# Optimization experiments

Hardware: AMD Instinct MI355X
Metric: run time of the kernel (lower is better)

The kernel has to match this reference:

```python
import jax, jax.numpy as jnp
import numpy as np

STRIDES = (8, 16, 32)
H = W = 640
SCORE_T = 0.5
NMS_T = 0.4


def setup_inputs() -> dict:
    key = jax.random.key(0)
    ks = jax.random.split(key, 9)
    feats = [(H // s) * (W // s) for s in STRIDES]  # 6400, 1600, 400
    d = {}
    for i, n in enumerate(feats):
        d[f"score{i}"] = jax.random.normal(ks[i], (1, n, 1), jnp.float32)
        d[f"bbox{i}"] = jax.random.normal(ks[3 + i], (1, n, 4), jnp.float32)
        d[f"kps{i}"] = jax.random.normal(ks[6 + i], (1, n, 10), jnp.float32)
    return d


def _anchors(stride):
    fh, fw = H // stride, W // stride
    yv, xv = jnp.meshgrid(jnp.arange(fh), jnp.arange(fw), indexing="ij")
    return jnp.stack([xv, yv], -1).reshape(-1, 2).astype(jnp.float32) * stride


def _decode(score, bbox, kps, stride):
    pts = _anchors(stride)                      # [N,2]
    s = jax.nn.sigmoid(score[0]).reshape(-1)    # [N]
    d = bbox[0] * stride                        # [N,4]
    x1 = pts[:, 0] - d[:, 0]
    y1 = pts[:, 1] - d[:, 1]
    x2 = pts[:, 0] + d[:, 2]
    y2 = pts[:, 1] + d[:, 3]
    b = jnp.stack([x1, y1, x2, y2], -1)         # [N,4]
    kd = (kps[0] * stride).reshape(-1, 5, 2)    # [N,5,2] (px,py pairs)
    k = (pts[:, None, :] + kd).reshape(-1, 10)  # [N,10]
    return s, b, k


def _iou(b):
    area = (b[:, 2] - b[:, 0]) * (b[:, 3] - b[:, 1])
    lt = jnp.maximum(b[:, None, :2], b[None, :, :2])
    rb = jnp.minimum(b[:, None, 2:], b[None, :, 2:])
    wh = jnp.clip(rb - lt, 0.0)
    inter = wh[..., 0] * wh[..., 1]
    return inter / (area[:, None] + area[None, :] - inter + 1e-9)


def _nms_keep(iou, valid, thresh):
    # greedy NMS on score-sorted boxes: keep i iff no earlier kept j has IoU>thresh
    n = valid.shape[0]
    def body(keep, xs):
        i, row = xs
        suppressed = jnp.any(keep & (row > thresh))
        keep = keep.at[i].set(valid[i] & ~suppressed)
        return keep, None
    keep, _ = jax.lax.scan(body, jnp.zeros(n, bool), (jnp.arange(n), iou))
    return keep


def reference(score0, score1, score2, bbox0, bbox1, bbox2, kps0, kps1, kps2):
    parts = [
        _decode(s, b, k, st)
        for s, b, k, st in zip(
            (score0, score1, score2), (bbox0, bbox1, bbox2), (kps0, kps1, kps2), STRIDES
        )
    ]
    scores = jnp.concatenate([p[0] for p in parts])  # [8400]
    boxes = jnp.concatenate([p[1] for p in parts])   # [8400,4]
    kpss = jnp.concatenate([p[2] for p in parts])    # [8400,10]
    order = jnp.argsort(-scores)                     # score-descending (NMS order)
    scores = scores[order]
    boxes = boxes[order]
    kpss = kpss[order]
    valid = scores > SCORE_T                         # threshold mask
    iou = _iou(jax.lax.stop_gradient(boxes))         # [8400,8400] ~282MB
    keep = _nms_keep(iou, valid, NMS_T)
    m = keep.astype(boxes.dtype)
    # fixed-shape equivalent of dynamic gather: suppressed rows zeroed, keep mask returned
    return boxes * m[:, None], scores * m, kpss * m[:, None], keep
```

## Files before the change

kernel.cpp:

```cpp
#include <hip/hip_runtime.h>
#include <math.h>

#define N_TOT 8400
#define MASK_WORDS 132
#define CAP 32
#define RT 33

typedef unsigned long long u64;

__device__ __forceinline__ unsigned mono_u32(float f) {
    unsigned u = __float_as_uint(f);
    return (u & 0x80000000u) ? ~u : (u | 0x80000000u);
}

__global__ void decode_kernel(const float* __restrict__ score0, const float* __restrict__ bbox0, const float* __restrict__ kps0,
                              const float* __restrict__ score1, const float* __restrict__ bbox1, const float* __restrict__ kps1,
                              const float* __restrict__ score2, const float* __restrict__ bbox2, const float* __restrict__ kps2,
                              float* __restrict__ logit, float* __restrict__ sig,
                              float* __restrict__ box, float* __restrict__ kps,
                              u64* __restrict__ key, int* __restrict__ rank,
                              unsigned int* __restrict__ cnt,
                              u64* __restrict__ validw, u64* __restrict__ rowflag) {
    int i = blockIdx.x * blockDim.x + threadIdx.x;
    if (i >= N_TOT) return;
    if (i < MASK_WORDS) { validw[i] = 0ull; rowflag[i] = 0ull; }
    rank[i] = 0;
    cnt[i] = 0u;
    const float *sc, *bb, *kp;
    int m, F; float s;
    if (i < 6400)      { sc = score0; bb = bbox0; kp = kps0; m = i;        F = 80; s = 8.f;  }
    else if (i < 8000) { sc = score1; bb = bbox1; kp = kps1; m = i - 6400; F = 40; s = 16.f; }
    else               { sc = score2; bb = bbox2; kp = kps2; m = i - 8000; F = 20; s = 32.f; }
    float px = (float)(m % F) * s;
    float py = (float)(m / F) * s;
    float lg = sc[m];
    logit[i] = lg;
    sig[i] = 1.0f / (1.0f + expf(-lg));
    key[i] = ((u64)(~mono_u32(lg)) << 14) | (u64)i;
    float d0 = bb[m*4+0]*s, d1 = bb[m*4+1]*s, d2 = bb[m*4+2]*s, d3 = bb[m*4+3]*s;
    box[i*4+0] = px - d0;
    box[i*4+1] = py - d1;
    box[i*4+2] = px + d2;
    box[i*4+3] = py + d3;
    #pragma unroll
    for (int c = 0; c < 5; ++c) {
        kps[i*10 + 2*c]   = px + kp[m*10 + 2*c]   * s;
        kps[i*10 + 2*c+1] = py + kp[m*10 + 2*c+1] * s;
    }
}

__global__ __launch_bounds__(256) void rank_kernel(const u64* __restrict__ key, int* __restrict__ rank) {
    __shared__ u64 tile[256];
    int i = blockIdx.x * 256 + threadIdx.x;
    int t0 = blockIdx.y * 256;
    u64 ki = (i < N_TOT) ? key[i] : 0ull;
    int j = t0 + threadIdx.x;
    tile[threadIdx.x] = (j < N_TOT) ? key[j] : ~0ull;
    __syncthreads();
    if (i >= N_TOT) return;
    int rk = 0;
    #pragma unroll 8
    for (int k = 0; k < 256; ++k) {
        rk += (tile[k] < ki) ? 1 : 0;
    }
    if (rk) atomicAdd(&rank[i], rk);
}

__global__ void scatter_kernel(const int* __restrict__ rank,
                               const float* __restrict__ logit, const float* __restrict__ sig,
                               const float* __restrict__ box, const float* __restrict__ kps,
                               float* __restrict__ s_logit, float* __restrict__ s_sig,
                               float* __restrict__ s_box, float* __restrict__ s_kps,
                               u64* __restrict__ validw) {
    int i = blockIdx.x * blockDim.x + threadIdx.x;
    if (i >= N_TOT) return;
    int r = rank[i];
    float lg = logit[i];
    s_logit[r] = lg;
    s_sig[r] = sig[i];
    #pragma unroll
    for (int c = 0; c < 4; ++c)  s_box[r*4+c] = box[i*4+c];
    #pragma unroll
    for (int c = 0; c < 10; ++c) s_kps[r*10+c] = kps[i*10+c];
    if (lg > 0.f) atomicOr(&validw[r >> 6], 1ull << (r & 63));
}

__global__ __launch_bounds__(64) void pairs_kernel(const float* __restrict__ s_logit,
                                                   const float* __restrict__ s_box,
                                                   unsigned int* __restrict__ cnt,
                                                   ulonglong2* __restrict__ ent,
                                                   u64* __restrict__ rowflag) {
    int cw = blockIdx.x;
    int rb = blockIdx.y;
    if (cw < rb) return;
    int tid = threadIdx.x;

    __shared__ float4 cbox[64];
    __shared__ float  carea[64];
    int j0 = cw * 64;
    int j = j0 + tid;
    float4 cb = make_float4(0.f, 0.f, 0.f, 0.f);
    float lgj = -1.f;
    if (j < N_TOT) {
        cb = ((const float4*)s_box)[j];
        lgj = s_logit[j];
    }
    cbox[tid] = cb;
    carea[tid] = (cb.z - cb.x) * (cb.w - cb.y);
    u64 cvalid = __ballot(j < N_TOT && lgj > 0.f);
    __syncthreads();
    if (cvalid == 0ull) return;

    int r = rb * 64 + tid;
    float lgr = (r < N_TOT) ? s_logit[r] : -1.f;
    if (__ballot(lgr > 0.f) == 0ull) return;

    u64 bits = 0ull;
    if (lgr > 0.f) {
        float4 rb4 = ((const float4*)s_box)[r];
        float rarea = (rb4.z - rb4.x) * (rb4.w - rb4.y);
        #pragma unroll 4
        for (int k = 0; k < 64; ++k) {
            float4 c4 = cbox[k];
            float ltx = fmaxf(rb4.x, c4.x);
            float lty = fmaxf(rb4.y, c4.y);
            float rbx = fminf(rb4.z, c4.z);
            float rby = fminf(rb4.w, c4.w);
            float w = fmaxf(rbx - ltx, 0.f);
            float h = fmaxf(rby - lty, 0.f);
            float inter = w * h;
            float iou = inter / (rarea + carea[k] - inter + 1e-9f);
            bits |= (iou > 0.4f) ? (1ull << k) : 0ull;
        }
        u64 m = cvalid;
        if (cw == rb) m &= (tid == 63) ? 0ull : (~0ull << (tid + 1));
        bits &= m;
    }
    if (bits) {
        unsigned idx = atomicAdd(&cnt[r], 1u);
        if (idx < CAP) {
            ulonglong2 e; e.x = bits; e.y = (u64)cw;
            ent[(size_t)r * CAP + idx] = e;
        }
        atomicOr(&rowflag[r >> 6], 1ull << (r & 63));
    }
}

__global__ __launch_bounds__(64) void nms_kernel(const u64* __restrict__ rowflag_g,
                                                 const u64* __restrict__ validw_g,
                                                 const unsigned int* __restrict__ cnt_g,
                                                 const ulonglong2* __restrict__ ent_g,
                                                 u64* __restrict__ keep_words) {
    __shared__ unsigned short list[8448];
    int lane = threadIdx.x;

    u64 rf[3], vw[3];
    #pragma unroll
    for (int s = 0; s < 3; ++s) {
        int w = s * 64 + lane;
        rf[s] = (w < MASK_WORDS) ? rowflag_g[w] : 0ull;
        vw[s] = (w < MASK_WORDS) ? validw_g[w] : 0ull;
    }

    int base = 0;
    #pragma unroll
    for (int s = 0; s < 3; ++s) {
        int c = (int)__popcll(rf[s]);
        int x = c;
        #pragma unroll
        for (int o = 1; o < 64; o <<= 1) { int y = __shfl_up(x, o); if (lane >= o) x += y; }
        int excl = x - c;
        int total = __shfl(x, 63);
        int off = base + excl;
        u64 t = rf[s];
        int wbase = (s * 64 + lane) << 6;
        while (t) {
            int b = __builtin_ctzll(t); t &= t - 1;
            list[off++] = (unsigned short)(wbase | b);
        }
        base += total;
    }
    int n_nz = base;
    __syncthreads();

    u64 rem0 = 0ull, rem1 = 0ull, rem2 = 0ull;

    if (n_nz > 0) {
        int half = lane >> 5;
        int sub  = lane & 31;

        int idx0 = min(sub, n_nz - 1);
        int rowCur = list[idx0];
        unsigned cntCur = cnt_g[rowCur];
        ulonglong2 entCur = ent_g[(size_t)rowCur * CAP + half];

        for (int k0 = 0; k0 < n_nz; k0 += 32) {
            int nb = k0 + 32;
            int rowNxt = 0; unsigned cntNxt = 0u;
            ulonglong2 entNxt; entNxt.x = 0ull; entNxt.y = 0ull;
            if (nb < n_nz) {
                int idx = min(nb + sub, n_nz - 1);
                rowNxt = list[idx];
                cntNxt = cnt_g[rowNxt];
                entNxt = ent_g[(size_t)rowNxt * CAP + half];
            }

            int lim = min(32, n_nz - k0);
            for (int i = 0; i < lim; ++i) {
                int r = __builtin_amdgcn_readlane(rowCur, i);
                int w = r >> 6, slot = w >> 6, owner = w & 63, b = r & 63;
                u64 rw = (slot == 0) ? rem0 : ((slot == 1) ? rem1 : rem2);
                unsigned halfw = (b < 32) ? (unsigned)rw : (unsigned)(rw >> 32);
                unsigned word = (unsigned)__builtin_amdgcn_readlane((int)halfw, owner);
                if (!((word >> (b & 31)) & 1u)) {
                    unsigned c = (unsigned)__builtin_amdgcn_readlane((int)cntCur, i);
                    int ec = (int)min(c, 2u);
                    for (int e = 0; e < ec; ++e) {
                        int src = e * 32 + i;
                        unsigned ey  = (unsigned)__builtin_amdgcn_readlane((int)(unsigned)entCur.y, src);
                        unsigned blo = (unsigned)__builtin_amdgcn_readlane((int)(unsigned)entCur.x, src);
                        unsigned bhi = (unsigned)__builtin_amdgcn_readlane((int)(unsigned)(entCur.x >> 32), src);
                        u64 bits = ((u64)bhi << 32) | (u64)blo;
                        int es = (int)(ey >> 6), eo = (int)(ey & 63u);
                        u64 add = (lane == eo) ? bits : 0ull;
                        if (es == 0) rem0 |= add; else if (es == 1) rem1 |= add; else rem2 |= add;
                    }
                    if (c > 2u) {
                        unsigned cm = min(c, (unsigned)CAP);
                        for (unsigned e = 2; e < cm; ++e) {
                            ulonglong2 g = ent_g[(size_t)r * CAP + e];
                            int es = (int)(g.y >> 6), eo = (int)(g.y & 63u);
                            u64 add = (lane == eo) ? g.x : 0ull;
                            if (es == 0) rem0 |= add; else if (es == 1) rem1 |= add; else rem2 |= add;
                        }
                    }
                }
            }
            rowCur = rowNxt; cntCur = cntNxt; entCur = entNxt;
        }
    }

    u64 rem[3] = {rem0, rem1, rem2};
    #pragma unroll
    for (int s = 0; s < 3; ++s) {
        int w = s * 64 + lane;
        if (w < MASK_WORDS) keep_words[w] = vw[s] & ~rem[s];
    }
}

__global__ void output_kernel(const float* __restrict__ s_sig, const float* __restrict__ s_box,
                              const float* __restrict__ s_kps,
                              const u64* __restrict__ keep_words,
                              float* __restrict__ out) {
    int r = blockIdx.x * blockDim.x + threadIdx.x;
    if (r >= N_TOT) return;
    float m = ((keep_words[r >> 6] >> (r & 63)) & 1ull) ? 1.0f : 0.0f;
    float* ob = out;
    float* os = out + 33600;
    float* okp = out + 42000;
    float* om = out + 126000;
    #pragma unroll
    for (int c = 0; c < 4; ++c)  ob[r*4+c] = s_box[r*4+c] * m;
    os[r] = s_sig[r] * m;
    #pragma unroll
    for (int c = 0; c < 10; ++c) okp[r*10+c] = s_kps[r*10+c] * m;
    om[r] = m;
}

extern "C" void kernel_launch(void* const* d_in, const int* in_sizes, int n_in,
                              void* d_out, int out_size, void* d_ws, size_t ws_size,
                              hipStream_t stream) {
    const float *score0, *bbox0, *kps0, *score1, *bbox1, *kps1, *score2, *bbox2, *kps2;
    if (in_sizes[1] == 25600) {
        score0 = (const float*)d_in[0]; bbox0 = (const float*)d_in[1]; kps0 = (const float*)d_in[2];
        score1 = (const float*)d_in[3]; bbox1 = (const float*)d_in[4]; kps1 = (const float*)d_in[5];
        score2 = (const float*)d_in[6]; bbox2 = (const float*)d_in[7]; kps2 = (const float*)d_in[8];
    } else {
        score0 = (const float*)d_in[0]; score1 = (const float*)d_in[1]; score2 = (const float*)d_in[2];
        bbox0  = (const float*)d_in[3]; bbox1  = (const float*)d_in[4]; bbox2  = (const float*)d_in[5];
        kps0   = (const float*)d_in[6]; kps1   = (const float*)d_in[7]; kps2   = (const float*)d_in[8];
    }

    char* ws = (char*)d_ws;
    float* logit   = (float*)(ws + 0);
    float* sig     = (float*)(ws + 33600);
    float* box     = (float*)(ws + 67200);
    float* kps     = (float*)(ws + 201600);
    int*   rank    = (int*)  (ws + 537600);
    float* s_logit = (float*)(ws + 571200);
    float* s_sig   = (float*)(ws + 604800);
    float* s_box   = (float*)(ws + 638400);
    float* s_kps   = (float*)(ws + 772800);
    u64*   keep_words = (u64*)(ws + 1108800);
    u64*   validw     = (u64*)(ws + 1110144);
    u64*   rowflag    = (u64*)(ws + 1111296);
    unsigned int* cnt = (unsigned int*)(ws + 1112448);
    u64*   key        = (u64*)(ws + 1146368);
    ulonglong2*   ent = (ulonglong2*)(ws + 1213568);

    float* out = (float*)d_out;

    decode_kernel<<<(N_TOT + 255) / 256, 256, 0, stream>>>(
        score0, bbox0, kps0, score1, bbox1, kps1, score2, bbox2, kps2,
        logit, sig, box, kps, key, rank, cnt, validw, rowflag);
    rank_kernel<<<dim3(RT, RT), 256, 0, stream>>>(key, rank);
    scatter_kernel<<<33, 256, 0, stream>>>(rank, logit, sig, box, kps,
                                           s_logit, s_sig, s_box, s_kps, validw);
    pairs_kernel<<<dim3(MASK_WORDS, MASK_WORDS), 64, 0, stream>>>(s_logit, s_box, cnt, ent, rowflag);
    nms_kernel<<<1, 64, 0, stream>>>(rowflag, validw, cnt, ent, keep_words);
    output_kernel<<<33, 256, 0, stream>>>(s_sig, s_box, s_kps, keep_words, out);
}
```

Baseline: 108.0 us.

## Process NMS per 64-row word with LDS removal mask and fold pairs grid

The pairs kernel now uses a folded triangular grid of about half the size, so blocks below the diagonal no longer launch only to exit. The single-wave NMS kernel changes from walking flagged rows one at a time with readlane broadcasts to walking whole 64-row words. All lanes test their row together and resolve in-word suppression with a short serial loop only when needed. Cross-word suppression goes into an LDS removal mask through atomicOr, with two words prefetched ahead. This adds a __syncthreads per word and LDS atomics.

New measurement: 113.5 us. +5.0%, slower.

```diff
diff --git a/kernel.cpp b/kernel.cpp
--- a/kernel.cpp
+++ b/kernel.cpp
@@ -90,9 +90,14 @@
                                                    unsigned int* __restrict__ cnt,
                                                    ulonglong2* __restrict__ ent,
                                                    u64* __restrict__ rowflag) {
-    int cw = blockIdx.x;
-    int rb = blockIdx.y;
-    if (cw < rb) return;
+    int x = blockIdx.x;
+    int y = blockIdx.y;
+    int rb, cw;
+    if (x + y < MASK_WORDS) { rb = x; cw = x + y; }
+    else {
+        if (y == MASK_WORDS / 2) return;
+        rb = x + y - MASK_WORDS; cw = x;
+    }
     int tid = threadIdx.x;
 
     __shared__ float4 cbox[64];
@@ -151,7 +156,8 @@
                                                  const unsigned int* __restrict__ cnt_g,
                                                  const ulonglong2* __restrict__ ent_g,
                                                  u64* __restrict__ keep_words) {
-    __shared__ unsigned short list[8448];
+    __shared__ u64 rem_lds[MASK_WORDS];
+    __shared__ unsigned short wlist[MASK_WORDS];
     int lane = threadIdx.x;
 
     u64 rf[3], vw[3];
@@ -160,91 +166,97 @@
         int w = s * 64 + lane;
         rf[s] = (w < MASK_WORDS) ? rowflag_g[w] : 0ull;
         vw[s] = (w < MASK_WORDS) ? validw_g[w] : 0ull;
+        if (w < MASK_WORDS) rem_lds[w] = 0ull;
     }
 
     int base = 0;
     #pragma unroll
     for (int s = 0; s < 3; ++s) {
-        int c = (int)__popcll(rf[s]);
-        int x = c;
-        #pragma unroll
-        for (int o = 1; o < 64; o <<= 1) { int y = __shfl_up(x, o); if (lane >= o) x += y; }
-        int excl = x - c;
-        int total = __shfl(x, 63);
-        int off = base + excl;
-        u64 t = rf[s];
-        int wbase = (s * 64 + lane) << 6;
-        while (t) {
-            int b = __builtin_ctzll(t); t &= t - 1;
-            list[off++] = (unsigned short)(wbase | b);
-        }
-        base += total;
-    }
-    int n_nz = base;
+        bool nz = rf[s] != 0ull;
+        u64 bal = __ballot(nz);
+        int pos = __popcll(bal & ((1ull << lane) - 1ull));
+        if (nz) wlist[base + pos] = (unsigned short)(s * 64 + lane);
+        base += (int)__popcll(bal);
+    }
+    int n_w = base;
     __syncthreads();
 
-    u64 rem0 = 0ull, rem1 = 0ull, rem2 = 0ull;
-
-    if (n_nz > 0) {
-        int half = lane >> 5;
-        int sub  = lane & 31;
-
-        int idx0 = min(sub, n_nz - 1);
-        int rowCur = list[idx0];
-        unsigned cntCur = cnt_g[rowCur];
-        ulonglong2 entCur = ent_g[(size_t)rowCur * CAP + half];
-
-        for (int k0 = 0; k0 < n_nz; k0 += 32) {
-            int nb = k0 + 32;
-            int rowNxt = 0; unsigned cntNxt = 0u;
-            ulonglong2 entNxt; entNxt.x = 0ull; entNxt.y = 0ull;
-            if (nb < n_nz) {
-                int idx = min(nb + sub, n_nz - 1);
-                rowNxt = list[idx];
-                cntNxt = cnt_g[rowNxt];
-                entNxt = ent_g[(size_t)rowNxt * CAP + half];
-            }
-
-            int lim = min(32, n_nz - k0);
-            for (int i = 0; i < lim; ++i) {
-                int r = __builtin_amdgcn_readlane(rowCur, i);
-                int w = r >> 6, slot = w >> 6, owner = w & 63, b = r & 63;
-                u64 rw = (slot == 0) ? rem0 : ((slot == 1) ? rem1 : rem2);
-                unsigned halfw = (b < 32) ? (unsigned)rw : (unsigned)(rw >> 32);
-                unsigned word = (unsigned)__builtin_amdgcn_readlane((int)halfw, owner);
-                if (!((word >> (b & 31)) & 1u)) {
-                    unsigned c = (unsigned)__builtin_amdgcn_readlane((int)cntCur, i);
-                    int ec = (int)min(c, 2u);
-                    for (int e = 0; e < ec; ++e) {
-                        int src = e * 32 + i;
-                        unsigned ey  = (unsigned)__builtin_amdgcn_readlane((int)(unsigned)entCur.y, src);
-                        unsigned blo = (unsigned)__builtin_amdgcn_readlane((int)(unsigned)entCur.x, src);
-                        unsigned bhi = (unsigned)__builtin_amdgcn_readlane((int)(unsigned)(entCur.x >> 32), src);
-                        u64 bits = ((u64)bhi << 32) | (u64)blo;
-                        int es = (int)(ey >> 6), eo = (int)(ey & 63u);
-                        u64 add = (lane == eo) ? bits : 0ull;
-                        if (es == 0) rem0 |= add; else if (es == 1) rem1 |= add; else rem2 |= add;
-                    }
-                    if (c > 2u) {
-                        unsigned cm = min(c, (unsigned)CAP);
-                        for (unsigned e = 2; e < cm; ++e) {
-                            ulonglong2 g = ent_g[(size_t)r * CAP + e];
-                            int es = (int)(g.y >> 6), eo = (int)(g.y & 63u);
-                            u64 add = (lane == eo) ? g.x : 0ull;
-                            if (es == 0) rem0 |= add; else if (es == 1) rem1 |= add; else rem2 |= add;
-                        }
+    auto LOADW = [&](int t, int &wd, unsigned &c, ulonglong2 &e0, ulonglong2 &e1, u64 &lb) {
+        wd = 0; c = 0u; e0.x = 0ull; e0.y = 0ull; e1.x = 0ull; e1.y = 0ull; lb = 0ull;
+        if (t < n_w) {
+            wd = (int)wlist[t];
+            int row = wd * 64 + lane;
+            if (row < N_TOT) {
+                c = cnt_g[row];
+                if (c > 0u) { e0 = ent_g[(size_t)row * CAP];     if ((int)e0.y == wd) lb |= e0.x; }
+                if (c > 1u) { e1 = ent_g[(size_t)row * CAP + 1]; if ((int)e1.y == wd) lb |= e1.x; }
+                if (c > 2u) {
+                    unsigned cm = min(c, (unsigned)CAP);
+                    for (unsigned e = 2; e < cm; ++e) {
+                        ulonglong2 g = ent_g[(size_t)row * CAP + e];
+                        if ((int)g.y == wd) lb |= g.x;
                     }
                 }
             }
-            rowCur = rowNxt; cntCur = cntNxt; entCur = entNxt;
         }
-    }
-
-    u64 rem[3] = {rem0, rem1, rem2};
+    };
+
+    int wA, wB; unsigned cA, cB; ulonglong2 eA0, eA1, eB0, eB1; u64 lbA, lbB;
+    LOADW(0, wA, cA, eA0, eA1, lbA);
+    LOADW(1, wB, cB, eB0, eB1, lbB);
+
+    for (int t = 0; t < n_w; ++t) {
+        int wC; unsigned cC; ulonglong2 eC0, eC1; u64 lbC;
+        LOADW(t + 2, wC, cC, eC0, eC1, lbC);
+
+        __syncthreads();
+        u64 remw = rem_lds[wA];
+        u64 cand = __ballot(cA > 0u) & ~remw;
+        if (cand) {
+            u64 kept;
+            u64 localmask = __ballot(lbA != 0ull) & cand;
+            if (localmask == 0ull) {
+                kept = cand;
+            } else {
+                kept = 0ull;
+                u64 remw_new = remw;
+                u64 pend = cand;
+                while (pend) {
+                    int b = __builtin_ctzll(pend);
+                    pend &= pend - 1ull;
+                    if (!((remw_new >> b) & 1ull)) {
+                        kept |= 1ull << b;
+                        unsigned lo = (unsigned)__builtin_amdgcn_readlane((int)(unsigned)lbA, b);
+                        unsigned hi = (unsigned)__builtin_amdgcn_readlane((int)(unsigned)(lbA >> 32), b);
+                        remw_new |= ((u64)hi << 32) | (u64)lo;
+                        pend &= ~remw_new;
+                    }
+                }
+                if (lane == 0) rem_lds[wA] = remw_new;
+            }
+            if ((kept >> lane) & 1ull) {
+                if (cA > 0u) { int yw = (int)eA0.y; if (yw != wA) atomicOr(&rem_lds[yw], eA0.x); }
+                if (cA > 1u) { int yw = (int)eA1.y; if (yw != wA) atomicOr(&rem_lds[yw], eA1.x); }
+                if (cA > 2u) {
+                    unsigned cm = min(cA, (unsigned)CAP);
+                    int row = wA * 64 + lane;
+                    for (unsigned e = 2; e < cm; ++e) {
+                        ulonglong2 g = ent_g[(size_t)row * CAP + e];
+                        int yw = (int)g.y;
+                        if (yw != wA) atomicOr(&rem_lds[yw], g.x);
+                    }
+                }
+            }
+        }
+        wA = wB; cA = cB; eA0 = eB0; eA1 = eB1; lbA = lbB;
+        wB = wC; cB = cC; eB0 = eC0; eB1 = eC1; lbB = lbC;
+    }
+
+    __syncthreads();
     #pragma unroll
     for (int s = 0; s < 3; ++s) {
         int w = s * 64 + lane;
-        if (w < MASK_WORDS) keep_words[w] = vw[s] & ~rem[s];
+        if (w < MASK_WORDS) keep_words[w] = vw[s] & ~rem_lds[w];
     }
 }
 
@@ -306,7 +318,7 @@
     rank_kernel<<<dim3(RT, RT), 256, 0, stream>>>(key, rank);
     scatter_kernel<<<33, 256, 0, stream>>>(rank, logit, sig, box, kps,
                                            s_logit, s_sig, s_box, s_kps, validw);
-    pairs_kernel<<<dim3(MASK_WORDS, MASK_WORDS), 64, 0, stream>>>(s_logit, s_box, cnt, ent, rowflag);
+    pairs_kernel<<<dim3(MASK_WORDS, MASK_WORDS / 2 + 1), 64, 0, stream>>>(s_logit, s_box, cnt, ent, rowflag);
     nms_kernel<<<1, 64, 0, stream>>>(rowflag, validw, cnt, ent, keep_words);
     output_kernel<<<33, 256, 0, stream>>>(s_sig, s_box, s_kps, keep_words, out);
 }
```
